# Kernel optimization log

Measured on AMD Instinct MI355X. Metric: run time of the kernel, lower is better.

The kernel has to match this reference:

```python
import jax, jax.numpy as jnp
import numpy as np

N_USER = 1_000_000
N_ITEM = 100_000
E = 16          # embedding_size
O = 16          # out_size per head
H = 4           # head_num
HID = 32        # hidden_size
B = 8192        # batch
S = 200         # sample_num
L = 50          # history length
NSUPP = 50_000  # supp_user_num


def _xavier(key, shape):
    fan_in, fan_out = shape[-2], shape[-1]
    std = np.sqrt(2.0 / (fan_in + fan_out))
    return (jax.random.normal(key, shape) * std).astype(jnp.float32)


def setup_inputs() -> dict:
    key = jax.random.key(0)
    ks = jax.random.split(key, 16)
    uid = jax.random.randint(ks[0], (B,), 0, N_USER)
    iid = jax.random.randint(ks[1], (B,), 0, N_ITEM)
    return {
        "user_embedding": _xavier(ks[2], (N_USER, E)),
        "item_embedding": _xavier(ks[3], (N_ITEM, E)),
        "wq": _xavier(ks[4], (H, E, O)),   # per-head Wq (no bias)
        "wk": _xavier(ks[5], (H, E, O)),
        "wv": _xavier(ks[6], (H, O, O)),
        "w_out": _xavier(ks[7], (H * O, O)),
        "l1_w": _xavier(ks[8], (3 * E, HID)),
        "l1_b": jnp.full((HID,), 0.1, jnp.float32),
        "l2_w": _xavier(ks[9], (HID, HID // 2)),
        "l2_b": jnp.full((HID // 2,), 0.1, jnp.float32),
        "l3_w": _xavier(ks[10], (HID // 2, 1)),
        "l3_b": jnp.full((1,), 0.1, jnp.float32),
        "user_bias": jnp.zeros((N_USER, 1), jnp.float32),
        "item_bias": jnp.zeros((N_ITEM, 1), jnp.float32),
        "x": jnp.stack([uid, iid], axis=1),                          # [B,2]
        "history": jax.random.randint(ks[11], (B, L), 0, N_ITEM),    # [B,L]
        "history_len": jax.random.randint(ks[12], (B,), 1, L + 1),   # [B] >=1
        "supp_users": jax.random.randint(ks[13], (NSUPP,), 0, N_USER),
        "sample_index": jax.random.randint(ks[14], (H, B, S), 0, NSUPP),
    }


def reference(user_embedding, item_embedding, wq, wk, wv, w_out,
              l1_w, l1_b, l2_w, l2_b, l3_w, l3_b, user_bias, item_bias,
              x, history, history_len, supp_users, sample_index):
    user_id = x[:, 0]
    item_id = x[:, 1]

    # user init embedding = mean-by-len of full (unmasked) history, as in source
    hist_emb = item_embedding[history]                                # [B,L,E]
    user_init = hist_emb.sum(axis=1) / history_len[:, None].astype(jnp.float32)  # [B,E]

    # per-head GAT over sampled support users (all heads vectorized)
    nb = user_embedding[supp_users[sample_index]]                     # [H,B,S,E]
    q = jnp.einsum('be,heo->hbo', user_init, wq)                      # [H,B,O]
    k = jnp.einsum('hbse,heo->hbso', nb, wk)                          # [H,B,S,O]
    attn = jax.nn.softmax(jnp.einsum('hbo,hbso->hbs', q, k), axis=-1)
    ctx = jnp.einsum('hbs,hbso->hbo', attn, k)                        # [H,B,O]
    gat = jnp.einsum('hbo,hop->hbp', ctx, wv)                         # [H,B,O]
    gat = jnp.transpose(gat, (1, 0, 2)).reshape(B, H * O)             # concat heads

    user_emb = gat @ w_out                                            # [B,O]
    item_emb = item_embedding[item_id]                                # [B,E]
    interaction = user_emb * item_emb
    ratings = interaction.sum(axis=1)

    h = jnp.concatenate([user_emb, item_emb, interaction], axis=1)    # [B,3E]
    x1 = jnp.tanh(h @ l1_w + l1_b)
    x2 = jnp.tanh(x1 @ l2_w + l2_b)
    x3 = (x2 @ l3_w + l3_b).reshape(-1)

    ub = user_bias[user_id, 0]
    ib = item_bias[item_id, 0]
    return (ratings + x3) / 2.0 + ub + ib
```

## Files before the change

### kernel.cpp

```cpp
#include <hip/hip_runtime.h>
#include <math.h>

#define N_USERS 1000000
#define N_ITEMS 100000
#define EMB 16
#define OUTD 16
#define NH 4
#define HID 32
#define BB 8192
#define SS 200
#define LL 50
#define NSUPP 50000

typedef float v4f __attribute__((ext_vector_type(4)));

__global__ __launch_bounds__(256) void k_supp_kernel(
    const float* __restrict__ user_emb,
    const int*   __restrict__ supp_users,
    const float* __restrict__ wk,
    float*       __restrict__ Ksupp)
{
    __shared__ float s_wk[NH * EMB * OUTD];
    __shared__ float s_u[16][EMB];
    int t = threadIdx.x;
    for (int i = t; i < NH * EMB * OUTD; i += 256) s_wk[i] = wk[i];
    int n0 = blockIdx.x * 16;
    {
        int ul = t >> 4, e = t & 15;
        int row = supp_users[n0 + ul];
        s_u[ul][e] = user_emb[(size_t)row * EMB + e];
    }
    __syncthreads();
    int h   = t >> 6;
    int sub = (t >> 4) & 3;
    int o   = t & 15;
#pragma unroll
    for (int r = 0; r < 4; ++r) {
        int ul = sub + 4 * r;
        float acc = 0.f;
#pragma unroll
        for (int e = 0; e < EMB; ++e)
            acc += s_u[ul][e] * s_wk[(h * EMB + e) * OUTD + o];
        Ksupp[((size_t)h * NSUPP + n0 + ul) * OUTD + o] = acc;
    }
}

__global__ __launch_bounds__(256) void user_init_q_kernel(
    const float* __restrict__ item_emb,
    const int*   __restrict__ history,
    const int*   __restrict__ history_len,
    const float* __restrict__ wq,
    float*       __restrict__ qbuf)
{
    __shared__ float s_ui[4][EMB];
    __shared__ float s_wq[NH * EMB * OUTD];
    int t = threadIdx.x;
    for (int i = t; i < NH * EMB * OUTD; i += 256) s_wq[i] = wq[i];

    int g    = t >> 6;
    int lane = t & 63;
    int l4   = lane >> 4;
    int e    = lane & 15;
    int b    = blockIdx.x * 4 + g;

    float sum = 0.f;
    for (int l = l4; l < LL; l += 4) {
        int it = __builtin_nontemporal_load(history + (size_t)b * LL + l);
        sum += item_emb[(size_t)it * EMB + e];
    }
    sum += __shfl_xor(sum, 16);
    sum += __shfl_xor(sum, 32);
    if (lane < EMB) s_ui[g][lane] = sum / (float)history_len[b];
    __syncthreads();

    int h  = (t >> 4) & 3;
    int o  = t & 15;
    float acc = 0.f;
#pragma unroll
    for (int ee = 0; ee < EMB; ++ee)
        acc += s_ui[g][ee] * s_wq[(h * EMB + ee) * OUTD + o];
    qbuf[((size_t)b * NH + h) * OUTD + o] = acc;
}

__global__ __launch_bounds__(256, 4) void attn_kernel(
    const float* __restrict__ Ksupp,
    const float* __restrict__ qbuf,
    const int*   __restrict__ sample_index,
    const float* __restrict__ wv,
    float*       __restrict__ gat)
{
    int blk   = blockIdx.x;
    int h     = (blk & 7) >> 1;
    int btile = ((blk >> 3) << 1) | (blk & 1);
    int wave  = threadIdx.x >> 6;
    int lane  = threadIdx.x & 63;
    int b     = btile * 4 + wave;
    int g     = lane >> 2;
    int qt    = lane & 3;

    const int* si = sample_index + ((size_t)h * BB + b) * SS;
    int pre0 = __builtin_nontemporal_load(si + lane);
    int pre1 = __builtin_nontemporal_load(si + lane + 64);
    int pre2 = __builtin_nontemporal_load(si + lane + 128);
    int pre3 = (lane < 8) ? __builtin_nontemporal_load(si + lane + 192) : 0;

    v4f qv = __builtin_nontemporal_load(
        (const v4f*)(qbuf + ((size_t)b * NH + h) * OUTD) + qt);

    const float* Kh = Ksupp + (size_t)h * NSUPP * OUTD;

    int idx[13];
#pragma unroll
    for (int r = 0; r < 13; ++r) {
        int pre = (r < 4) ? pre0 : (r < 8) ? pre1 : (r < 12) ? pre2 : pre3;
        idx[r] = __shfl(pre, (r & 3) * 16 + g, 64);
    }

    v4f kq[13];
#pragma unroll
    for (int r = 0; r < 13; ++r)
        kq[r] = *(const v4f*)(Kh + (size_t)idx[r] * OUTD + qt * 4);

    float d[13];
#pragma unroll
    for (int r = 0; r < 13; ++r) {
        float p = kq[r].x * qv.x + kq[r].y * qv.y + kq[r].z * qv.z + kq[r].w * qv.w;
        p += __shfl_xor(p, 1);
        p += __shfl_xor(p, 2);
        d[r] = p;
    }
    if (g >= 8) d[12] = -3.0e38f;

    float m = d[0];
#pragma unroll
    for (int r = 1; r < 13; ++r) m = fmaxf(m, d[r]);
#pragma unroll
    for (int off = 4; off < 64; off <<= 1) m = fmaxf(m, __shfl_xor(m, off));

    float l = 0.f;
    v4f c = {0.f, 0.f, 0.f, 0.f};
#pragma unroll
    for (int r = 0; r < 13; ++r) {
        float w = __expf(d[r] - m);
        l += w;
        c += w * kq[r];
    }
#pragma unroll
    for (int off = 4; off < 64; off <<= 1) {
        l   += __shfl_xor(l, off);
        c.x += __shfl_xor(c.x, off);
        c.y += __shfl_xor(c.y, off);
        c.z += __shfl_xor(c.z, off);
        c.w += __shfl_xor(c.w, off);
    }
    float inv = 1.f / l;

    float part = c.x * wv[((size_t)h * OUTD + qt * 4 + 0) * OUTD + g]
               + c.y * wv[((size_t)h * OUTD + qt * 4 + 1) * OUTD + g]
               + c.z * wv[((size_t)h * OUTD + qt * 4 + 2) * OUTD + g]
               + c.w * wv[((size_t)h * OUTD + qt * 4 + 3) * OUTD + g];
    part += __shfl_xor(part, 1);
    part += __shfl_xor(part, 2);
    if (qt == 0)
        gat[(size_t)b * (NH * OUTD) + h * OUTD + g] = part * inv;
}

__global__ __launch_bounds__(256) void epilogue_kernel(
    const float* __restrict__ gat,
    const float* __restrict__ item_emb,
    const float* __restrict__ w_out,
    const float* __restrict__ l1_w, const float* __restrict__ l1_b,
    const float* __restrict__ l2_w, const float* __restrict__ l2_b,
    const float* __restrict__ l3_w, const float* __restrict__ l3_b,
    const float* __restrict__ user_bias, const float* __restrict__ item_bias,
    const int*   __restrict__ x,
    float*       __restrict__ out)
{
    int t    = threadIdx.x;
    int g    = t >> 6;
    int lane = t & 63;
    int b    = blockIdx.x * 4 + g;

    __shared__ float s_gat[4][NH * OUTD];
    __shared__ float s_ue[4][OUTD];
    __shared__ float s_ie[4][EMB];
    __shared__ float s_x1[4][HID];
    __shared__ float s_x2[4][HID / 2];

    int uid = x[(size_t)b * 2 + 0];
    int iid = x[(size_t)b * 2 + 1];

    s_gat[g][lane] = gat[(size_t)b * (NH * OUTD) + lane];
    if (lane < EMB) s_ie[g][lane] = item_emb[(size_t)iid * EMB + lane];
    __syncthreads();

    if (lane < OUTD) {
        float acc = 0.f;
#pragma unroll
        for (int j = 0; j < NH * OUTD; ++j) acc += s_gat[g][j] * w_out[j * OUTD + lane];
        s_ue[g][lane] = acc;
    }
    __syncthreads();

    if (lane < HID) {
        float acc = l1_b[lane];
#pragma unroll
        for (int i = 0; i < EMB; ++i) {
            float ue = s_ue[g][i], ie = s_ie[g][i];
            acc += ue * l1_w[i * HID + lane]
                 + ie * l1_w[(EMB + i) * HID + lane]
                 + ue * ie * l1_w[(2 * EMB + i) * HID + lane];
        }
        s_x1[g][lane] = tanhf(acc);
    }
    __syncthreads();

    if (lane < HID / 2) {
        float acc = l2_b[lane];
#pragma unroll
        for (int j = 0; j < HID; ++j) acc += s_x1[g][j] * l2_w[j * (HID / 2) + lane];
        s_x2[g][lane] = tanhf(acc);
    }
    __syncthreads();

    if (lane == 0) {
        float x3 = l3_b[0];
#pragma unroll
        for (int j = 0; j < HID / 2; ++j) x3 += s_x2[g][j] * l3_w[j];
        float ratings = 0.f;
#pragma unroll
        for (int o = 0; o < OUTD; ++o) ratings += s_ue[g][o] * s_ie[g][o];
        out[b] = 0.5f * (ratings + x3) + user_bias[uid] + item_bias[iid];
    }
}

extern "C" void kernel_launch(void* const* d_in, const int* in_sizes, int n_in,
                              void* d_out, int out_size, void* d_ws, size_t ws_size,
                              hipStream_t stream) {
    const float* user_embedding = (const float*)d_in[0];
    const float* item_embedding = (const float*)d_in[1];
    const float* wq             = (const float*)d_in[2];
    const float* wk             = (const float*)d_in[3];
    const float* wv             = (const float*)d_in[4];
    const float* w_out          = (const float*)d_in[5];
    const float* l1_w           = (const float*)d_in[6];
    const float* l1_b           = (const float*)d_in[7];
    const float* l2_w           = (const float*)d_in[8];
    const float* l2_b           = (const float*)d_in[9];
    const float* l3_w           = (const float*)d_in[10];
    const float* l3_b           = (const float*)d_in[11];
    const float* user_bias      = (const float*)d_in[12];
    const float* item_bias      = (const float*)d_in[13];
    const int*   x              = (const int*)d_in[14];
    const int*   history        = (const int*)d_in[15];
    const int*   history_len    = (const int*)d_in[16];
    const int*   supp_users     = (const int*)d_in[17];
    const int*   sample_index   = (const int*)d_in[18];
    float* out = (float*)d_out;

    char* ws = (char*)d_ws;
    float* Ksupp = (float*)ws;
    ws += (size_t)NH * NSUPP * OUTD * sizeof(float);
    float* qbuf  = (float*)ws;
    ws += (size_t)BB * NH * OUTD * sizeof(float);
    float* gat   = (float*)ws;

    k_supp_kernel<<<NSUPP / 16, 256, 0, stream>>>(user_embedding, supp_users, wk, Ksupp);
    user_init_q_kernel<<<BB / 4, 256, 0, stream>>>(item_embedding, history, history_len, wq, qbuf);
    attn_kernel<<<NH * BB / 4, 256, 0, stream>>>(Ksupp, qbuf, sample_index, wv, gat);
    epilogue_kernel<<<BB / 4, 256, 0, stream>>>(
        gat, item_embedding, w_out, l1_w, l1_b, l2_w, l2_b, l3_w, l3_b,
        user_bias, item_bias, x, out);
}
```

Baseline: 213.3 us.

## Store projected keys in fp16, drop softmax max pass, merge prep kernels

Result: slower. 220.1 us (+3.2%).

```diff
diff --git a/kernel.cpp b/kernel.cpp
--- a/kernel.cpp
+++ b/kernel.cpp
@@ -13,77 +13,77 @@
 #define NSUPP 50000
 
 typedef float v4f __attribute__((ext_vector_type(4)));
-
-__global__ __launch_bounds__(256) void k_supp_kernel(
+typedef _Float16 h4 __attribute__((ext_vector_type(4)));
+typedef _Float16 h2 __attribute__((ext_vector_type(2)));
+
+__global__ __launch_bounds__(256) void prep_kernel(
     const float* __restrict__ user_emb,
     const int*   __restrict__ supp_users,
     const float* __restrict__ wk,
-    float*       __restrict__ Ksupp)
-{
-    __shared__ float s_wk[NH * EMB * OUTD];
-    __shared__ float s_u[16][EMB];
-    int t = threadIdx.x;
-    for (int i = t; i < NH * EMB * OUTD; i += 256) s_wk[i] = wk[i];
-    int n0 = blockIdx.x * 16;
-    {
-        int ul = t >> 4, e = t & 15;
-        int row = supp_users[n0 + ul];
-        s_u[ul][e] = user_emb[(size_t)row * EMB + e];
-    }
-    __syncthreads();
-    int h   = t >> 6;
-    int sub = (t >> 4) & 3;
-    int o   = t & 15;
-#pragma unroll
-    for (int r = 0; r < 4; ++r) {
-        int ul = sub + 4 * r;
-        float acc = 0.f;
-#pragma unroll
-        for (int e = 0; e < EMB; ++e)
-            acc += s_u[ul][e] * s_wk[(h * EMB + e) * OUTD + o];
-        Ksupp[((size_t)h * NSUPP + n0 + ul) * OUTD + o] = acc;
-    }
-}
-
-__global__ __launch_bounds__(256) void user_init_q_kernel(
+    _Float16*    __restrict__ Ksupp,
     const float* __restrict__ item_emb,
     const int*   __restrict__ history,
     const int*   __restrict__ history_len,
     const float* __restrict__ wq,
     float*       __restrict__ qbuf)
 {
+    __shared__ float s_wk[NH * EMB * OUTD];
+    __shared__ float s_u[16][EMB];
     __shared__ float s_ui[4][EMB];
     __shared__ float s_wq[NH * EMB * OUTD];
+
     int t = threadIdx.x;
-    for (int i = t; i < NH * EMB * OUTD; i += 256) s_wq[i] = wq[i];
-
-    int g    = t >> 6;
-    int lane = t & 63;
-    int l4   = lane >> 4;
-    int e    = lane & 15;
-    int b    = blockIdx.x * 4 + g;
-
-    float sum = 0.f;
-    for (int l = l4; l < LL; l += 4) {
-        int it = __builtin_nontemporal_load(history + (size_t)b * LL + l);
-        sum += item_emb[(size_t)it * EMB + e];
-    }
-    sum += __shfl_xor(sum, 16);
-    sum += __shfl_xor(sum, 32);
-    if (lane < EMB) s_ui[g][lane] = sum / (float)history_len[b];
-    __syncthreads();
-
-    int h  = (t >> 4) & 3;
-    int o  = t & 15;
-    float acc = 0.f;
-#pragma unroll
-    for (int ee = 0; ee < EMB; ++ee)
-        acc += s_ui[g][ee] * s_wq[(h * EMB + ee) * OUTD + o];
-    qbuf[((size_t)b * NH + h) * OUTD + o] = acc;
-}
-
-__global__ __launch_bounds__(256, 4) void attn_kernel(
-    const float* __restrict__ Ksupp,
+    if (blockIdx.x < NSUPP / 16) {
+        for (int i = t; i < NH * EMB * OUTD; i += 256) s_wk[i] = wk[i];
+        int n0 = blockIdx.x * 16;
+        {
+            int ul = t >> 4, e = t & 15;
+            int row = supp_users[n0 + ul];
+            s_u[ul][e] = user_emb[(size_t)row * EMB + e];
+        }
+        __syncthreads();
+        int h   = t >> 6;
+        int sub = (t >> 4) & 3;
+        int o   = t & 15;
+#pragma unroll
+        for (int r = 0; r < 4; ++r) {
+            int ul = sub + 4 * r;
+            float acc = 0.f;
+#pragma unroll
+            for (int e = 0; e < EMB; ++e)
+                acc += s_u[ul][e] * s_wk[(h * EMB + e) * OUTD + o];
+            Ksupp[((size_t)h * NSUPP + n0 + ul) * OUTD + o] = (_Float16)acc;
+        }
+    } else {
+        for (int i = t; i < NH * EMB * OUTD; i += 256) s_wq[i] = wq[i];
+        int g    = t >> 6;
+        int lane = t & 63;
+        int l4   = lane >> 4;
+        int e    = lane & 15;
+        int b    = (blockIdx.x - NSUPP / 16) * 4 + g;
+
+        float sum = 0.f;
+        for (int l = l4; l < LL; l += 4) {
+            int it = __builtin_nontemporal_load(history + (size_t)b * LL + l);
+            sum += item_emb[(size_t)it * EMB + e];
+        }
+        sum += __shfl_xor(sum, 16);
+        sum += __shfl_xor(sum, 32);
+        if (lane < EMB) s_ui[g][lane] = sum / (float)history_len[b];
+        __syncthreads();
+
+        int h = (t >> 4) & 3;
+        int o = t & 15;
+        float acc = 0.f;
+#pragma unroll
+        for (int ee = 0; ee < EMB; ++ee)
+            acc += s_ui[g][ee] * s_wq[(h * EMB + ee) * OUTD + o];
+        qbuf[((size_t)b * NH + h) * OUTD + o] = acc;
+    }
+}
+
+__global__ __launch_bounds__(256, 8) void attn_kernel(
+    const _Float16* __restrict__ Ksupp,
     const float* __restrict__ qbuf,
     const int*   __restrict__ sample_index,
     const float* __restrict__ wv,
@@ -106,8 +106,11 @@
 
     v4f qv = __builtin_nontemporal_load(
         (const v4f*)(qbuf + ((size_t)b * NH + h) * OUTD) + qt);
-
-    const float* Kh = Ksupp + (size_t)h * NSUPP * OUTD;
+    h4 qh = __builtin_convertvector(qv, h4);
+    h2 qlo = {qh.x, qh.y};
+    h2 qhi = {qh.z, qh.w};
+
+    const h4* K4 = (const h4*)(Ksupp + (size_t)h * NSUPP * OUTD);
 
     int idx[13];
 #pragma unroll
@@ -116,34 +119,26 @@
         idx[r] = __shfl(pre, (r & 3) * 16 + g, 64);
     }
 
-    v4f kq[13];
+    h4 kq[13];
 #pragma unroll
     for (int r = 0; r < 13; ++r)
-        kq[r] = *(const v4f*)(Kh + (size_t)idx[r] * OUTD + qt * 4);
-
-    float d[13];
+        kq[r] = K4[idx[r] * 4 + qt];
+
+    float l = 0.f;
+    v4f c = {0.f, 0.f, 0.f, 0.f};
 #pragma unroll
     for (int r = 0; r < 13; ++r) {
-        float p = kq[r].x * qv.x + kq[r].y * qv.y + kq[r].z * qv.z + kq[r].w * qv.w;
+        h2 klo = {kq[r].x, kq[r].y};
+        h2 khi = {kq[r].z, kq[r].w};
+        float p = __builtin_amdgcn_fdot2(klo, qlo,
+                  __builtin_amdgcn_fdot2(khi, qhi, 0.f, false), false);
         p += __shfl_xor(p, 1);
         p += __shfl_xor(p, 2);
-        d[r] = p;
-    }
-    if (g >= 8) d[12] = -3.0e38f;
-
-    float m = d[0];
-#pragma unroll
-    for (int r = 1; r < 13; ++r) m = fmaxf(m, d[r]);
-#pragma unroll
-    for (int off = 4; off < 64; off <<= 1) m = fmaxf(m, __shfl_xor(m, off));
-
-    float l = 0.f;
-    v4f c = {0.f, 0.f, 0.f, 0.f};
-#pragma unroll
-    for (int r = 0; r < 13; ++r) {
-        float w = __expf(d[r] - m);
+        float w = __expf(p);
+        if (r == 12) w = (g < 8) ? w : 0.f;
         l += w;
-        c += w * kq[r];
+        v4f kf = __builtin_convertvector(kq[r], v4f);
+        c += w * kf;
     }
 #pragma unroll
     for (int off = 4; off < 64; off <<= 1) {
@@ -259,14 +254,15 @@
     float* out = (float*)d_out;
 
     char* ws = (char*)d_ws;
-    float* Ksupp = (float*)ws;
-    ws += (size_t)NH * NSUPP * OUTD * sizeof(float);
+    _Float16* Ksupp = (_Float16*)ws;
+    ws += (size_t)NH * NSUPP * OUTD * sizeof(_Float16);
     float* qbuf  = (float*)ws;
     ws += (size_t)BB * NH * OUTD * sizeof(float);
     float* gat   = (float*)ws;
 
-    k_supp_kernel<<<NSUPP / 16, 256, 0, stream>>>(user_embedding, supp_users, wk, Ksupp);
-    user_init_q_kernel<<<BB / 4, 256, 0, stream>>>(item_embedding, history, history_len, wq, qbuf);
+    prep_kernel<<<NSUPP / 16 + BB / 4, 256, 0, stream>>>(
+        user_embedding, supp_users, wk, Ksupp,
+        item_embedding, history, history_len, wq, qbuf);
     attn_kernel<<<NH * BB / 4, 256, 0, stream>>>(Ksupp, qbuf, sample_index, wv, gat);
     epilogue_kernel<<<BB / 4, 256, 0, stream>>>(
         gat, item_embedding, w_out, l1_w, l1_b, l2_w, l2_b, l3_w, l3_b,
```
